# Kernel optimization log

Measured on AMD Instinct MI355X. Metric: run time of the kernel, lower is better.

Reference implementation:

```python
import jax, jax.numpy as jnp
import numpy as np

N_NODES = 100000
N_EDGES = 1600000
N_CLASS = 45


def gcn_conv(x, W, b, src, dst, ew, n):
    # PyG GCNConv: add self-loops (weight 1), symmetric deg^-1/2 normalization,
    # linear transform, scatter-add aggregation into targets, then bias.
    loops = jnp.arange(n, dtype=src.dtype)
    s = jnp.concatenate([src, loops])
    d = jnp.concatenate([dst, loops])
    w = jnp.concatenate([ew, jnp.ones((n,), ew.dtype)])
    deg = jax.ops.segment_sum(w, d, num_segments=n)          # in-degree (weighted)
    dis = jnp.where(deg > 0, 1.0 / jnp.sqrt(deg), 0.0)      # deg^-1/2, 0 where deg==0
    norm = dis[s] * w * dis[d]                               # [E+n]
    h = x @ W                                                # [n, out]
    out = jax.ops.segment_sum(h[s] * norm[:, None], d, num_segments=n)
    return out + b


def setup_inputs() -> dict:
    key = jax.random.key(0)
    ks = jax.random.split(key, 6)
    x = jax.random.normal(ks[0], (N_NODES, N_CLASS), dtype=jnp.float32)
    edge_src = jax.random.randint(ks[1], (N_EDGES,), 0, N_NODES, dtype=jnp.int64 if jax.config.jax_enable_x64 else jnp.int32).astype(jnp.int32)
    edge_dst = jax.random.randint(ks[2], (N_EDGES,), 0, N_NODES, dtype=jnp.int64 if jax.config.jax_enable_x64 else jnp.int32).astype(jnp.int32)
    edge_w = jax.random.uniform(ks[3], (N_EDGES,), dtype=jnp.float32)
    W1 = jax.random.normal(ks[4], (N_CLASS, 32), dtype=jnp.float32) / np.sqrt(N_CLASS)
    b1 = jnp.zeros((32,), dtype=jnp.float32)
    W2 = jax.random.normal(ks[5], (32, 128), dtype=jnp.float32) / np.sqrt(32.0)
    b2 = jnp.zeros((128,), dtype=jnp.float32)
    return {"x": x, "edge_src": edge_src, "edge_dst": edge_dst, "edge_w": edge_w,
            "W1": W1, "b1": b1, "W2": W2, "b2": b2}


def reference(x, edge_src, edge_dst, edge_w, W1, b1, W2, b2):
    n = x.shape[0]
    h = jnp.tanh(gcn_conv(x, W1, b1, edge_src, edge_dst, edge_w, n))
    return gcn_conv(h, W2, b2, edge_src, edge_dst, edge_w, n)
```

## Files before the change

### kernel.cpp

```cpp
#include <hip/hip_runtime.h>
#include <hip/hip_fp16.h>
#include <math.h>

static constexpr int TPB = 256;
static constexpr int NPB_SHIFT = 8;
static constexpr int BCAP = 5120;
static constexpr int HCAP = 2816;
static constexpr int CSTRIDE = 2 * HCAP;
static constexpr int PCHUNK = 4096;
static constexpr int PF = 16;

__device__ __forceinline__ int p_src(unsigned p) { return (int)(p >> 15); }
__device__ __forceinline__ float p_w(unsigned p) {
  return __half2float(__ushort_as_half((unsigned short)(p & 0x7FFFu)));
}

struct h2x4 { __half2 a, b, c, d; };

__global__ void k_partition(const int* __restrict__ src, const int* __restrict__ dst,
                            const float* __restrict__ ew, int* __restrict__ bkcnt,
                            unsigned* __restrict__ ppk, unsigned char* __restrict__ pld,
                            int E, int NB) {
  __shared__ int lh[512];
  __shared__ int lbase[512];
  __shared__ int lcur[512];
  int tid = threadIdx.x;
  long long e0 = (long long)blockIdx.x * PCHUNK;
  int d[PCHUNK / TPB];
  unsigned pk[PCHUNK / TPB];
  for (int t = tid; t < NB; t += TPB) { lh[t] = 0; lcur[t] = 0; }
  __syncthreads();
#pragma unroll
  for (int r = 0; r < PCHUNK / TPB; ++r) {
    long long e = e0 + (long long)r * TPB + tid;
    if (e < E) {
      d[r] = dst[e];
      pk[r] = ((unsigned)src[e] << 15) |
              ((unsigned)__half_as_ushort(__float2half(ew[e])) & 0x7FFFu);
      atomicAdd(&lh[d[r] >> NPB_SHIFT], 1);
    } else {
      d[r] = -1;
    }
  }
  __syncthreads();
  for (int t = tid; t < NB; t += TPB)
    lbase[t] = lh[t] ? (t * BCAP + atomicAdd(&bkcnt[t], lh[t])) : 0;
  __syncthreads();
#pragma unroll
  for (int r = 0; r < PCHUNK / TPB; ++r) {
    if (d[r] >= 0) {
      int b = d[r] >> NPB_SHIFT;
      int pos = atomicAdd(&lcur[b], 1);
      size_t gp = (size_t)lbase[b] + pos;
      ppk[gp] = pk[r];
      pld[gp] = (unsigned char)(d[r] & 255);
    }
  }
}

__global__ void __launch_bounds__(TPB) k_bucket(const unsigned* __restrict__ ppk,
                                                const unsigned char* __restrict__ pld,
                                                const int* __restrict__ bkcnt,
                                                unsigned* __restrict__ csr,
                                                int2* __restrict__ rc,
                                                float* __restrict__ dis,
                                                const float* __restrict__ x,
                                                const float* __restrict__ W1,
                                                __half2* __restrict__ hh, int n) {
  __shared__ float sW[45 * 32];
  __shared__ int lcnt[128];
  __shared__ int lofs[128];
  __shared__ float lsum[128];
  int b = blockIdx.x >> 1;
  int half = blockIdx.x & 1;
  int t = threadIdx.x;
  int beg = b * BCAP;
  int cbeg = b * CSTRIDE + half * HCAP;
  int m = bkcnt[b];
  if (m > BCAP) m = BCAP;
  if (t < 128) { lcnt[t] = 0; lsum[t] = 0.f; }
  for (int i = t; i < 45 * 32; i += TPB) sW[i] = W1[i];
  __syncthreads();
  for (int i = t; i < m; i += TPB) {
    int ld = pld[(size_t)beg + i];
    if ((ld >> 7) == half) atomicAdd(&lcnt[ld & 127], 1);
  }
  __syncthreads();
  int v = (t < 128) ? lcnt[t] : 0;
  if (t < 128) lofs[t] = v;
  __syncthreads();
  for (int off = 1; off < 128; off <<= 1) {
    int tv = (t < 128 && t >= off) ? lofs[t - off] : 0;
    __syncthreads();
    if (t < 128) lofs[t] += tv;
    __syncthreads();
  }
  int gnode = (b << NPB_SHIFT) + half * 128 + t;
  if (t < 128) {
    int ex = lofs[t] - v;
    if (gnode < n) rc[gnode] = make_int2(cbeg + ex, v);
    lcnt[t] = ex;
  }
  __syncthreads();
  for (int i = t; i < m; i += TPB) {
    int ld = pld[(size_t)beg + i];
    if ((ld >> 7) == half) {
      unsigned pk = ppk[(size_t)beg + i];
      int pos = atomicAdd(&lcnt[ld & 127], 1);
      csr[(size_t)cbeg + pos] = pk;
      atomicAdd(&lsum[ld & 127], p_w(pk));
    }
  }
  __syncthreads();
  int ln = t >> 1;
  int jh = t & 1;
  int gnode2 = (b << NPB_SHIFT) + half * 128 + ln;
  if (gnode2 < n) {
    float dsc = rsqrtf(1.0f + lsum[ln]);
    if (jh == 0) dis[gnode2] = dsc;
    float xr[45];
#pragma unroll
    for (int k = 0; k < 45; ++k) xr[k] = x[(size_t)gnode2 * 45 + k];
    __half2* hw = hh + (size_t)gnode2 * 16 + jh * 8;
#pragma unroll
    for (int j2 = 0; j2 < 8; ++j2) {
      int j = jh * 16 + j2 * 2;
      float a0 = 0.f, a1 = 0.f;
#pragma unroll
      for (int k = 0; k < 45; ++k) {
        a0 = fmaf(xr[k], sW[k * 32 + j], a0);
        a1 = fmaf(xr[k], sW[k * 32 + j + 1], a1);
      }
      hw[j2] = __floats2half2_rn(a0 * dsc, a1 * dsc);
    }
  }
}

#define ACC_EDGE(pk, cc0, cc1, cc2, cc3)                                             \
  {                                                                                  \
    h2x4 v = *reinterpret_cast<const h2x4*>(tbl + (size_t)p_src(pk) * 16);           \
    float w = p_w(pk);                                                               \
    float2 f;                                                                        \
    f = __half22float2(v.a); cc0.x = fmaf(w, f.x, cc0.x); cc0.y = fmaf(w, f.y, cc0.y); \
    f = __half22float2(v.b); cc1.x = fmaf(w, f.x, cc1.x); cc1.y = fmaf(w, f.y, cc1.y); \
    f = __half22float2(v.c); cc2.x = fmaf(w, f.x, cc2.x); cc2.y = fmaf(w, f.y, cc2.y); \
    f = __half22float2(v.d); cc3.x = fmaf(w, f.x, cc3.x); cc3.y = fmaf(w, f.y, cc3.y); \
  }

#define GATHER_CORE()                                                                \
  float2 c0 = {0.f, 0.f}, c1 = {0.f, 0.f}, c2 = {0.f, 0.f}, c3 = {0.f, 0.f};        \
  float2 d0 = {0.f, 0.f}, d1 = {0.f, 0.f}, d2 = {0.f, 0.f}, d3 = {0.f, 0.f};        \
  unsigned pr[PF];                                                                   \
  _Pragma("unroll") for (int i = 0; i < PF; ++i) { if (i < m) pr[i] = row[i]; }      \
  _Pragma("unroll") for (int i = 0; i < PF; ++i) {                                   \
    if (i < m) {                                                                     \
      if (i & 1) { ACC_EDGE(pr[i], d0, d1, d2, d3) }                                 \
      else       { ACC_EDGE(pr[i], c0, c1, c2, c3) }                                 \
    }                                                                                \
  }                                                                                  \
  int e = PF;                                                                        \
  for (; e + 3 < m; e += 4) {                                                        \
    unsigned p0 = row[e], p1 = row[e + 1], p2 = row[e + 2], p3 = row[e + 3];         \
    ACC_EDGE(p0, c0, c1, c2, c3)                                                     \
    ACC_EDGE(p1, d0, d1, d2, d3)                                                     \
    ACC_EDGE(p2, c0, c1, c2, c3)                                                     \
    ACC_EDGE(p3, d0, d1, d2, d3)                                                     \
  }                                                                                  \
  for (; e < m; ++e) { unsigned p = row[e]; ACC_EDGE(p, c0, c1, c2, c3) }            \
  c0.x += d0.x; c0.y += d0.y; c1.x += d1.x; c1.y += d1.y;                            \
  c2.x += d2.x; c2.y += d2.y; c3.x += d3.x; c3.y += d3.y;

template <bool TANH>
__global__ void k_gather(const unsigned* __restrict__ csr, const int2* __restrict__ rc,
                         const float* __restrict__ dis, const __half2* __restrict__ hh,
                         const float* __restrict__ b1, __half2* __restrict__ outv, int n) {
  int gid = blockIdx.x * blockDim.x + threadIdx.x;
  int node = gid >> 2;
  if (node >= n) return;
  int q = (threadIdx.x & 3) * 4;
  int2 r = rc[node];
  const unsigned* row = csr + r.x;
  int m = r.y;
  const __half2* tbl = hh + q;
  GATHER_CORE()
  float dd = dis[node];
  h2x4 own = *reinterpret_cast<const h2x4*>(hh + (size_t)node * 16 + q);
  __half2* op = outv + (size_t)node * 16 + q;
  float2 o0 = __half22float2(own.a), o1 = __half22float2(own.b);
  float2 o2 = __half22float2(own.c), o3 = __half22float2(own.d);
  if (TANH) {
    const float4* bp = reinterpret_cast<const float4*>(b1 + q * 2);
    float4 ba = bp[0], bb = bp[1];
    op[0] = __floats2half2_rn(dd * tanhf(ba.x + dd * (c0.x + o0.x)),
                              dd * tanhf(ba.y + dd * (c0.y + o0.y)));
    op[1] = __floats2half2_rn(dd * tanhf(ba.z + dd * (c1.x + o1.x)),
                              dd * tanhf(ba.w + dd * (c1.y + o1.y)));
    op[2] = __floats2half2_rn(dd * tanhf(bb.x + dd * (c2.x + o2.x)),
                              dd * tanhf(bb.y + dd * (c2.y + o2.y)));
    op[3] = __floats2half2_rn(dd * tanhf(bb.z + dd * (c3.x + o3.x)),
                              dd * tanhf(bb.w + dd * (c3.y + o3.y)));
  } else {
    op[0] = __floats2half2_rn(dd * (c0.x + o0.x), dd * (c0.y + o0.y));
    op[1] = __floats2half2_rn(dd * (c1.x + o1.x), dd * (c1.y + o1.y));
    op[2] = __floats2half2_rn(dd * (c2.x + o2.x), dd * (c2.y + o2.y));
    op[3] = __floats2half2_rn(dd * (c3.x + o3.x), dd * (c3.y + o3.y));
  }
}

__global__ void __launch_bounds__(TPB, 2)
k_gemm2r(const __half2* __restrict__ y, const float* __restrict__ W2,
         const float* __restrict__ b2, float* __restrict__ out, int n) {
  int lane = threadIdx.x & 63;
  int wid = (blockIdx.x * blockDim.x + threadIdx.x) >> 6;
  int nw = (gridDim.x * blockDim.x) >> 6;
  int c0 = lane * 2;
  float wr0[32], wr1[32];
#pragma unroll
  for (int k = 0; k < 32; ++k) {
    float2 wv = *reinterpret_cast<const float2*>(W2 + k * 128 + c0);
    wr0[k] = wv.x; wr1[k] = wv.y;
  }
  float2 bb = *reinterpret_cast<const float2*>(b2 + c0);

#define GEMM_NODE(node, ox, oy)                                                      \
  {                                                                                  \
    const h2x4* yr = reinterpret_cast<const h2x4*>(y + (size_t)(node) * 16);         \
    h2x4 yv[4] = {yr[0], yr[1], yr[2], yr[3]};                                       \
    _Pragma("unroll") for (int g = 0; g < 4; ++g) {                                  \
      __half2 hs[4] = {yv[g].a, yv[g].b, yv[g].c, yv[g].d};                          \
      _Pragma("unroll") for (int i = 0; i < 4; ++i) {                                \
        float2 f = __half22float2(hs[i]);                                            \
        ox = fmaf(f.x, wr0[g * 8 + i * 2], ox);                                      \
        oy = fmaf(f.x, wr1[g * 8 + i * 2], oy);                                      \
        ox = fmaf(f.y, wr0[g * 8 + i * 2 + 1], ox);                                  \
        oy = fmaf(f.y, wr1[g * 8 + i * 2 + 1], oy);                                  \
      }                                                                              \
    }                                                                                \
  }

  int node = wid * 2;
  int stride = nw * 2;
  for (; node + 1 < n; node += stride) {
    float a0 = bb.x, a1 = bb.y, b0 = bb.x, b1v = bb.y;
    GEMM_NODE(node, a0, a1)
    GEMM_NODE(node + 1, b0, b1v)
    *reinterpret_cast<float2*>(out + (size_t)node * 128 + c0) = make_float2(a0, a1);
    *reinterpret_cast<float2*>(out + (size_t)(node + 1) * 128 + c0) = make_float2(b0, b1v);
  }
  if (node < n) {
    float a0 = bb.x, a1 = bb.y;
    GEMM_NODE(node, a0, a1)
    *reinterpret_cast<float2*>(out + (size_t)node * 128 + c0) = make_float2(a0, a1);
  }
#undef GEMM_NODE
}

static inline dim3 gx(long long work) { return dim3((unsigned)((work + TPB - 1) / TPB)); }

extern "C" void kernel_launch(void* const* d_in, const int* in_sizes, int n_in,
                              void* d_out, int out_size, void* d_ws, size_t ws_size,
                              hipStream_t stream) {
  const float* x   = (const float*)d_in[0];
  const int*   src = (const int*)d_in[1];
  const int*   dst = (const int*)d_in[2];
  const float* ew  = (const float*)d_in[3];
  const float* W1  = (const float*)d_in[4];
  const float* b1  = (const float*)d_in[5];
  const float* W2  = (const float*)d_in[6];
  const float* b2  = (const float*)d_in[7];
  float* out = (float*)d_out;

  const int n = in_sizes[0] / 45;
  const int E = in_sizes[1];
  const int NB = (n + 255) >> NPB_SHIFT;

  char* w = (char*)d_ws;
  size_t o = 0;
  auto alloc = [&](size_t bytes) { void* p = w + o; o += ((bytes + 255) & ~(size_t)255); return p; };
  int*           bkcnt = (int*)          alloc((size_t)NB * 4);
  unsigned*      ppk   = (unsigned*)     alloc((size_t)NB * BCAP * 4);
  unsigned char* pld   = (unsigned char*)alloc((size_t)NB * BCAP);
  unsigned*      csr   = (unsigned*)     alloc((size_t)NB * CSTRIDE * 4);
  int2*          rc    = (int2*)         alloc((size_t)n * 8);
  float*         dis   = (float*)        alloc((size_t)n * 4);
  __half2*       hh    = (__half2*)      alloc((size_t)n * 32 * 2);
  __half2*       ag1   = (__half2*)      alloc((size_t)n * 32 * 2);
  __half2*       yb    = (__half2*)      alloc((size_t)n * 32 * 2);

  const int PB = (E + PCHUNK - 1) / PCHUNK;

  hipMemsetAsync(bkcnt, 0, (size_t)NB * 4, stream);
  k_partition<<<PB, TPB, 0, stream>>>(src, dst, ew, bkcnt, ppk, pld, E, NB);
  k_bucket<<<NB * 2, TPB, 0, stream>>>(ppk, pld, bkcnt, csr, rc, dis, x, W1, hh, n);
  k_gather<true><<<gx((long long)n * 4), TPB, 0, stream>>>(csr, rc, dis, hh, b1, ag1, n);
  k_gather<false><<<gx((long long)n * 4), TPB, 0, stream>>>(csr, rc, dis, ag1, b1, yb, n);
  k_gemm2r<<<1024, TPB, 0, stream>>>(yb, W2, b2, out, n);
}
```

Baseline: 142.0 us.

## Use 128-node buckets and stage bucket edges in LDS for CSR build

Bucket granularity drops from 256 to 128 destination nodes, so each k_bucket block owns one whole bucket instead of two blocks each filtering half of a shared bucket. Each block loads its bucket's packed edges and local dst bytes into shared memory once, and the counting and scatter passes reuse them. This removes the duplicated global reads and half-filtering of the old scheme. In exchange the partition kernel keeps a 1024-entry histogram with twice as many buckets and global atomics, per-bucket capacity headroom is tighter (2816 slots for about 2048 expected edges), and the larger shared-memory footprint may lower occupancy.

```diff
diff --git a/kernel.cpp b/kernel.cpp
--- a/kernel.cpp
+++ b/kernel.cpp
@@ -3,10 +3,8 @@
 #include <math.h>
 
 static constexpr int TPB = 256;
-static constexpr int NPB_SHIFT = 8;
-static constexpr int BCAP = 5120;
-static constexpr int HCAP = 2816;
-static constexpr int CSTRIDE = 2 * HCAP;
+static constexpr int NPB_SHIFT = 7;
+static constexpr int BCAP = 2816;
 static constexpr int PCHUNK = 4096;
 static constexpr int PF = 16;
 
@@ -21,9 +19,9 @@
                             const float* __restrict__ ew, int* __restrict__ bkcnt,
                             unsigned* __restrict__ ppk, unsigned char* __restrict__ pld,
                             int E, int NB) {
-  __shared__ int lh[512];
-  __shared__ int lbase[512];
-  __shared__ int lcur[512];
+  __shared__ int lh[1024];
+  __shared__ int lbase[1024];
+  __shared__ int lcur[1024];
   int tid = threadIdx.x;
   long long e0 = (long long)blockIdx.x * PCHUNK;
   int d[PCHUNK / TPB];
@@ -53,7 +51,7 @@
       int pos = atomicAdd(&lcur[b], 1);
       size_t gp = (size_t)lbase[b] + pos;
       ppk[gp] = pk[r];
-      pld[gp] = (unsigned char)(d[r] & 255);
+      pld[gp] = (unsigned char)(d[r] & 127);
     }
   }
 }
@@ -67,23 +65,26 @@
                                                 const float* __restrict__ x,
                                                 const float* __restrict__ W1,
                                                 __half2* __restrict__ hh, int n) {
+  __shared__ unsigned lpk[BCAP];
+  __shared__ unsigned char lld[BCAP];
   __shared__ float sW[45 * 32];
   __shared__ int lcnt[128];
   __shared__ int lofs[128];
   __shared__ float lsum[128];
-  int b = blockIdx.x >> 1;
-  int half = blockIdx.x & 1;
+  int b = blockIdx.x;
   int t = threadIdx.x;
   int beg = b * BCAP;
-  int cbeg = b * CSTRIDE + half * HCAP;
   int m = bkcnt[b];
   if (m > BCAP) m = BCAP;
   if (t < 128) { lcnt[t] = 0; lsum[t] = 0.f; }
   for (int i = t; i < 45 * 32; i += TPB) sW[i] = W1[i];
   __syncthreads();
   for (int i = t; i < m; i += TPB) {
-    int ld = pld[(size_t)beg + i];
-    if ((ld >> 7) == half) atomicAdd(&lcnt[ld & 127], 1);
+    unsigned pk = ppk[(size_t)beg + i];
+    unsigned char ld = pld[(size_t)beg + i];
+    lpk[i] = pk;
+    lld[i] = ld;
+    atomicAdd(&lcnt[ld], 1);
   }
   __syncthreads();
   int v = (t < 128) ? lcnt[t] : 0;
@@ -95,26 +96,24 @@
     if (t < 128) lofs[t] += tv;
     __syncthreads();
   }
-  int gnode = (b << NPB_SHIFT) + half * 128 + t;
+  int gnode = (b << NPB_SHIFT) + t;
   if (t < 128) {
     int ex = lofs[t] - v;
-    if (gnode < n) rc[gnode] = make_int2(cbeg + ex, v);
+    if (gnode < n) rc[gnode] = make_int2(beg + ex, v);
     lcnt[t] = ex;
   }
   __syncthreads();
   for (int i = t; i < m; i += TPB) {
-    int ld = pld[(size_t)beg + i];
-    if ((ld >> 7) == half) {
-      unsigned pk = ppk[(size_t)beg + i];
-      int pos = atomicAdd(&lcnt[ld & 127], 1);
-      csr[(size_t)cbeg + pos] = pk;
-      atomicAdd(&lsum[ld & 127], p_w(pk));
-    }
+    unsigned pk = lpk[i];
+    int ld = lld[i];
+    int pos = atomicAdd(&lcnt[ld], 1);
+    csr[(size_t)beg + pos] = pk;
+    atomicAdd(&lsum[ld], p_w(pk));
   }
   __syncthreads();
   int ln = t >> 1;
   int jh = t & 1;
-  int gnode2 = (b << NPB_SHIFT) + half * 128 + ln;
+  int gnode2 = (b << NPB_SHIFT) + ln;
   if (gnode2 < n) {
     float dsc = rsqrtf(1.0f + lsum[ln]);
     if (jh == 0) dis[gnode2] = dsc;
@@ -272,7 +271,7 @@
 
   const int n = in_sizes[0] / 45;
   const int E = in_sizes[1];
-  const int NB = (n + 255) >> NPB_SHIFT;
+  const int NB = (n + 127) >> NPB_SHIFT;
 
   char* w = (char*)d_ws;
   size_t o = 0;
@@ -280,7 +279,7 @@
   int*           bkcnt = (int*)          alloc((size_t)NB * 4);
   unsigned*      ppk   = (unsigned*)     alloc((size_t)NB * BCAP * 4);
   unsigned char* pld   = (unsigned char*)alloc((size_t)NB * BCAP);
-  unsigned*      csr   = (unsigned*)     alloc((size_t)NB * CSTRIDE * 4);
+  unsigned*      csr   = (unsigned*)     alloc((size_t)NB * BCAP * 4);
   int2*          rc    = (int2*)         alloc((size_t)n * 8);
   float*         dis   = (float*)        alloc((size_t)n * 4);
   __half2*       hh    = (__half2*)      alloc((size_t)n * 32 * 2);
@@ -291,7 +290,7 @@
 
   hipMemsetAsync(bkcnt, 0, (size_t)NB * 4, stream);
   k_partition<<<PB, TPB, 0, stream>>>(src, dst, ew, bkcnt, ppk, pld, E, NB);
-  k_bucket<<<NB * 2, TPB, 0, stream>>>(ppk, pld, bkcnt, csr, rc, dis, x, W1, hh, n);
+  k_bucket<<<NB, TPB, 0, stream>>>(ppk, pld, bkcnt, csr, rc, dis, x, W1, hh, n);
   k_gather<true><<<gx((long long)n * 4), TPB, 0, stream>>>(csr, rc, dis, hh, b1, ag1, n);
   k_gather<false><<<gx((long long)n * 4), TPB, 0, stream>>>(csr, rc, dis, ag1, b1, yb, n);
   k_gemm2r<<<1024, TPB, 0, stream>>>(yb, W2, b2, out, n);
```

New measurement: 144.0 us. About the same (+1.4%).
